# Optimization experiments

Hardware: AMD Instinct MI355X
Metric: run time of the kernel (lower is better)

## Reference

```python
import jax, jax.numpy as jnp
import numpy as np
from jax import lax

B, N, D, H, E, K, FF = 4, 1024, 1024, 16, 12, 2, 4
HD = D // H
EPS_LN = 1e-5


def setup_inputs() -> dict:
    key = jax.random.key(0)
    ks = jax.random.split(key, 10)
    s = 0.02
    return {
        "x": jax.random.normal(ks[0], (B, N, D), jnp.float32),
        "Wr": jax.random.normal(ks[1], (E, D), jnp.float32) * s,          # router [E, D] (no bias)
        "Wq": jax.random.normal(ks[2], (E, D, D), jnp.float32) * s,       # per-expert [out, in]
        "Wk": jax.random.normal(ks[3], (E, D, D), jnp.float32) * s,
        "Wv": jax.random.normal(ks[4], (E, D, D), jnp.float32) * s,
        "Wo": jax.random.normal(ks[5], (E, D, D), jnp.float32) * s,
        "W1": jax.random.normal(ks[6], (FF * D, D), jnp.float32) * s,
        "b1": jnp.zeros((FF * D,), jnp.float32),
        "W2": jax.random.normal(ks[7], (D, FF * D), jnp.float32) * s,
        "b2": jnp.zeros((D,), jnp.float32),
        "g1": jnp.ones((D,), jnp.float32),
        "be1": jnp.zeros((D,), jnp.float32),
        "g2": jnp.ones((D,), jnp.float32),
        "be2": jnp.zeros((D,), jnp.float32),
    }


def _ln(x, g, b):
    m = jnp.mean(x, axis=-1, keepdims=True)
    v = jnp.mean(jnp.square(x - m), axis=-1, keepdims=True)
    return (x - m) * lax.rsqrt(v + EPS_LN) * g + b


def _moe_mix(inp, W, combine):
    """sum_e combine[:, e] * (inp @ W[e].T) via scan over the E experts.
    inp: [T, Din], W: [E, Dout, Din], combine: [T, E] -> [T, Dout]"""
    def body(acc, ec):
        We, ce = ec
        return acc + ce[:, None] * (inp @ We.T), None
    acc0 = jnp.zeros((inp.shape[0], W.shape[1]), inp.dtype)
    acc, _ = lax.scan(body, acc0, (W, jnp.swapaxes(combine, 0, 1)))
    return acc


def _moe_attention(x, Wr, Wq, Wk, Wv, Wo):
    x_flat = x.reshape(-1, D)                     # [T, D]
    T = x_flat.shape[0]
    logits = x_flat @ Wr.T                        # [T, E]
    probs = jax.nn.softmax(logits, axis=-1)
    topv, topi = lax.top_k(probs, K)              # [T, K]
    topv = topv / (jnp.sum(topv, axis=-1, keepdims=True) + 1e-6)
    # dense combine weights [T, E] (zero for unselected experts)
    combine = jnp.zeros((T, E), x.dtype).at[jnp.arange(T)[:, None], topi].add(topv)

    q = _moe_mix(x_flat, Wq, combine)
    k = _moe_mix(x_flat, Wk, combine)
    v = _moe_mix(x_flat, Wv, combine)

    # [B, H, N, HD]
    q = q.reshape(B, N, H, HD).transpose(0, 2, 1, 3)
    k = k.reshape(B, N, H, HD).transpose(0, 2, 1, 3)
    v = v.reshape(B, N, H, HD).transpose(0, 2, 1, 3)
    scores = jnp.einsum("bhqd,bhkd->bhqk", q, k) / jnp.sqrt(jnp.asarray(HD, x.dtype))
    attn = jax.nn.softmax(scores, axis=-1)
    out = jnp.einsum("bhqk,bhkd->bhqd", attn, v)
    out_flat = out.transpose(0, 2, 1, 3).reshape(T, D)

    o = _moe_mix(out_flat, Wo, combine)           # expert output projection

    # load-balance loss (no grad in original: computed under torch.no_grad)
    counts = jnp.zeros((E,), x.dtype).at[topi.ravel()].add(1.0)
    p = probs.sum(axis=0)
    lb = jax.lax.stop_gradient((counts / (counts.sum() + 1e-6) * p).sum() * E)
    return o.reshape(B, N, D), lb


def reference(x, Wr, Wq, Wk, Wv, Wo, W1, b1, W2, b2, g1, be1, g2, be2):
    # pre-norm transformer block: x + MoEAttn(LN(x)); + FFN(LN(.))
    attn_out, lb = _moe_attention(_ln(x, g1, be1), Wr, Wq, Wk, Wv, Wo)
    h = x + attn_out
    hn = _ln(h, g2, be2)
    ff = (jax.nn.gelu(hn @ W1.T + b1)) @ W2.T + b2   # dropout=0 (eval)
    y = h + ff
    return y, lb
```

## Files before the change

### kernel.cpp

```cpp
#include <hip/hip_runtime.h>

#define B_ 4
#define N_ 1024
#define D_ 1024
#define H_ 16
#define HD_ 64
#define E_ 12
#define T_ 4096
#define FF_ 4096

static constexpr size_t SZ_ = (size_t)T_ * D_;

typedef __attribute__((ext_vector_type(8))) short bhalf8;
typedef __attribute__((ext_vector_type(4))) float f32x4;

#define GLDS(gp, lp)                                                         \
  __builtin_amdgcn_global_load_lds(                                          \
      (const __attribute__((address_space(1))) void*)(gp),                   \
      (__attribute__((address_space(3))) void*)(lp), 16, 0, 0)

__device__ __forceinline__ float wave_sum64(float v) {
#pragma unroll
  for (int o = 32; o > 0; o >>= 1) v += __shfl_down(v, o);
  return v;
}

__device__ __forceinline__ unsigned short f2bf(float f) {
  unsigned u = __float_as_uint(f);
  u += 0x7FFFu + ((u >> 16) & 1u);
  return (unsigned short)(u >> 16);
}
__device__ __forceinline__ float b2f(unsigned short s) {
  return __uint_as_float(((unsigned)s) << 16);
}
__device__ __forceinline__ unsigned addpair_bf(unsigned x, unsigned y) {
  float lo = b2f((unsigned short)(x & 0xffff)) + b2f((unsigned short)(y & 0xffff));
  float hi = b2f((unsigned short)(x >> 16)) + b2f((unsigned short)(y >> 16));
  return (unsigned)f2bf(lo) | ((unsigned)f2bf(hi) << 16);
}

__device__ __forceinline__ float gelu_f(float x) {
  float u = 0.7978845608028654f * (x + 0.044715f * x * x * x);
  u = fminf(fmaxf(u, -15.f), 15.f);
  float e = __expf(2.f * u);
  float th = (e - 1.f) / (e + 1.f);
  return 0.5f * x * (1.f + th);
}

__device__ __forceinline__ int slot_of(int row, int q) {
  return row * 4 + (q ^ ((row >> 1) & 3));
}

__global__ __launch_bounds__(256) void ln_kernel(const float* __restrict__ x,
    const float* __restrict__ g, const float* __restrict__ b,
    unsigned short* __restrict__ outb) {
  const int t = blockIdx.x, tid = threadIdx.x;
  const size_t base = (size_t)t * D_;
  const float4 v = ((const float4*)(x + base))[tid];
  float s = v.x + v.y + v.z + v.w;
  float s2 = v.x * v.x + v.y * v.y + v.z * v.z + v.w * v.w;
  s = wave_sum64(s);
  s2 = wave_sum64(s2);
  __shared__ float ls[4], ls2[4];
  const int w = tid >> 6;
  if ((tid & 63) == 0) { ls[w] = s; ls2[w] = s2; }
  __syncthreads();
  const float mean = (ls[0] + ls[1] + ls[2] + ls[3]) * (1.0f / D_);
  const float var = (ls2[0] + ls2[1] + ls2[2] + ls2[3]) * (1.0f / D_) - mean * mean;
  const float inv = rsqrtf(var + 1e-5f);
  const float4 gg = ((const float4*)g)[tid];
  const float4 bb = ((const float4*)b)[tid];
  ushort4 u4;
  u4.x = f2bf((v.x - mean) * inv * gg.x + bb.x);
  u4.y = f2bf((v.y - mean) * inv * gg.y + bb.y);
  u4.z = f2bf((v.z - mean) * inv * gg.z + bb.z);
  u4.w = f2bf((v.w - mean) * inv * gg.w + bb.w);
  ((ushort4*)(outb + base))[tid] = u4;
}

__global__ __launch_bounds__(256) void hln2_kernel(const float* __restrict__ x,
    const unsigned short* __restrict__ oa, const unsigned short* __restrict__ ob,
    const float* __restrict__ g, const float* __restrict__ be,
    const float* __restrict__ b2, float* __restrict__ y,
    unsigned short* __restrict__ hnb) {
  const int t = blockIdx.x, tid = threadIdx.x;
  const size_t base = (size_t)t * D_;
  const float4 xv = ((const float4*)(x + base))[tid];
  const ushort4 av = ((const ushort4*)(oa + base))[tid];
  const ushort4 bv = ((const ushort4*)(ob + base))[tid];
  float4 hv;
  hv.x = xv.x + b2f(av.x) + b2f(bv.x);
  hv.y = xv.y + b2f(av.y) + b2f(bv.y);
  hv.z = xv.z + b2f(av.z) + b2f(bv.z);
  hv.w = xv.w + b2f(av.w) + b2f(bv.w);
  const float4 b2v = ((const float4*)b2)[tid];
  float4 yv;
  yv.x = hv.x + b2v.x; yv.y = hv.y + b2v.y;
  yv.z = hv.z + b2v.z; yv.w = hv.w + b2v.w;
  ((float4*)(y + base))[tid] = yv;
  float s = hv.x + hv.y + hv.z + hv.w;
  float s2 = hv.x * hv.x + hv.y * hv.y + hv.z * hv.z + hv.w * hv.w;
  s = wave_sum64(s);
  s2 = wave_sum64(s2);
  __shared__ float ls[4], ls2[4];
  const int w = tid >> 6;
  if ((tid & 63) == 0) { ls[w] = s; ls2[w] = s2; }
  __syncthreads();
  const float mean = (ls[0] + ls[1] + ls[2] + ls[3]) * (1.0f / D_);
  const float var = (ls2[0] + ls2[1] + ls2[2] + ls2[3]) * (1.0f / D_) - mean * mean;
  const float inv = rsqrtf(var + 1e-5f);
  const float4 gg = ((const float4*)g)[tid];
  const float4 bb = ((const float4*)be)[tid];
  ushort4 o4;
  o4.x = f2bf((hv.x - mean) * inv * gg.x + bb.x);
  o4.y = f2bf((hv.y - mean) * inv * gg.y + bb.y);
  o4.z = f2bf((hv.z - mean) * inv * gg.z + bb.z);
  o4.w = f2bf((hv.w - mean) * inv * gg.w + bb.w);
  ((ushort4*)(hnb + base))[tid] = o4;
}

__global__ __launch_bounds__(256) void router_ln(const float* __restrict__ x,
    const float* __restrict__ g, const float* __restrict__ b,
    const float* __restrict__ Wr, float* __restrict__ probs,
    int* __restrict__ topi, float2* __restrict__ topw) {
  const int t = blockIdx.x, tid = threadIdx.x;
  const float4 xv = ((const float4*)(x + (size_t)t * D_))[tid];
  float s = xv.x + xv.y + xv.z + xv.w;
  float s2 = xv.x * xv.x + xv.y * xv.y + xv.z * xv.z + xv.w * xv.w;
  s = wave_sum64(s);
  s2 = wave_sum64(s2);
  __shared__ float ls[4], ls2[4];
  const int w = tid >> 6;
  if ((tid & 63) == 0) { ls[w] = s; ls2[w] = s2; }
  __syncthreads();
  const float mean = (ls[0] + ls[1] + ls[2] + ls[3]) * (1.0f / D_);
  const float var = (ls2[0] + ls2[1] + ls2[2] + ls2[3]) * (1.0f / D_) - mean * mean;
  const float inv = rsqrtf(var + 1e-5f);
  const float4 gg = ((const float4*)g)[tid];
  const float4 bb = ((const float4*)b)[tid];
  float4 xn4;
  xn4.x = (xv.x - mean) * inv * gg.x + bb.x;
  xn4.y = (xv.y - mean) * inv * gg.y + bb.y;
  xn4.z = (xv.z - mean) * inv * gg.z + bb.z;
  xn4.w = (xv.w - mean) * inv * gg.w + bb.w;
  float acc[E_];
#pragma unroll
  for (int e = 0; e < E_; ++e) {
    const float4 wv = ((const float4*)(Wr + (size_t)e * D_))[tid];
    acc[e] = xn4.x * wv.x + xn4.y * wv.y + xn4.z * wv.z + xn4.w * wv.w;
  }
#pragma unroll
  for (int e = 0; e < E_; ++e) acc[e] = wave_sum64(acc[e]);
  __shared__ float red[4][E_];
  if ((tid & 63) == 0) {
#pragma unroll
    for (int e = 0; e < E_; ++e) red[w][e] = acc[e];
  }
  __syncthreads();
  if (tid == 0) {
    float lg[E_];
    float mx = -1e30f;
#pragma unroll
    for (int e = 0; e < E_; ++e) {
      lg[e] = red[0][e] + red[1][e] + red[2][e] + red[3][e];
      mx = fmaxf(mx, lg[e]);
    }
    float p[E_];
    float sum = 0.f;
#pragma unroll
    for (int e = 0; e < E_; ++e) { p[e] = __expf(lg[e] - mx); sum += p[e]; }
    const float invs = 1.f / sum;
#pragma unroll
    for (int e = 0; e < E_; ++e) {
      p[e] *= invs;
      probs[t * E_ + e] = p[e];
    }
    int i0 = 0;
#pragma unroll
    for (int e = 1; e < E_; ++e) if (p[e] > p[i0]) i0 = e;
    int i1 = (i0 == 0) ? 1 : 0;
#pragma unroll
    for (int e = 0; e < E_; ++e) if (e != i0 && p[e] > p[i1]) i1 = e;
    const float rs = 1.f / (p[i0] + p[i1] + 1e-6f);
    topi[t] = i0 | (i1 << 8);
    topw[t] = make_float2(p[i0] * rs, p[i1] * rs);
  }
}

__global__ __launch_bounds__(256) void psum_kernel(const float* __restrict__ probs,
                                                   float* __restrict__ psum) {
  const int tid = threadIdx.x;
  float local[E_] = {};
  for (int t = tid; t < T_; t += 256) {
#pragma unroll
    for (int e = 0; e < E_; ++e) local[e] += probs[t * E_ + e];
  }
#pragma unroll
  for (int e = 0; e < E_; ++e) local[e] = wave_sum64(local[e]);
  __shared__ float red[4][E_];
  const int w = tid >> 6;
  if ((tid & 63) == 0) {
#pragma unroll
    for (int e = 0; e < E_; ++e) red[w][e] = local[e];
  }
  __syncthreads();
  if (tid < E_)
    psum[tid] = red[0][tid] + red[1][tid] + red[2][tid] + red[3][tid];
}

__global__ __launch_bounds__(256) void build_lists(const int* __restrict__ topi,
    const float2* __restrict__ topw, int* __restrict__ ecnt,
    int* __restrict__ etok, float* __restrict__ ewt) {
  const int e = blockIdx.x;
  const int tid = threadIdx.x;
  const int wid = tid >> 6, lane = tid & 63;
  __shared__ int wbase[4];
  __shared__ int base;
  if (tid == 0) base = 0;
  __syncthreads();
  for (int c = 0; c < T_; c += 256) {
    const int t = c + tid;
    const int pk = topi[t];
    const int i0 = pk & 0xFF, i1 = (pk >> 8) & 0xFF;
    const float2 w2 = topw[t];
    const int sel = (i0 == e) ? 0 : ((i1 == e) ? 1 : -1);
    const unsigned long long mask = __ballot(sel >= 0);
    const int prefix = __popcll(mask & ((1ULL << lane) - 1ULL));
    if (lane == 0) wbase[wid] = __popcll(mask);
    __syncthreads();
    if (tid == 0) {
      int s = base;
#pragma unroll
      for (int ww = 0; ww < 4; ++ww) { int cc = wbase[ww]; wbase[ww] = s; s += cc; }
      base = s;
    }
    __syncthreads();
    if (sel >= 0) {
      const int pos = wbase[wid] + prefix;
      etok[e * T_ + pos] = t | (sel << 16);
      ewt[e * T_ + pos] = sel ? w2.y : w2.x;
    }
    __syncthreads();
  }
  if (tid == 0) ecnt[e] = base;
}

__global__ __launch_bounds__(256) void cvtw_kernel(const float* __restrict__ src,
    unsigned short* __restrict__ dst) {
  const size_t i = (size_t)blockIdx.x * 256 + threadIdx.x;
  const float4 v = ((const float4*)src)[i];
  ushort4 o;
  o.x = f2bf(v.x); o.y = f2bf(v.y); o.z = f2bf(v.z); o.w = f2bf(v.w);
  ((ushort4*)dst)[i] = o;
}

__global__ __launch_bounds__(256) void cvtw3_kernel(const float* __restrict__ a,
    const float* __restrict__ b, const float* __restrict__ c,
    unsigned short* __restrict__ dst) {
  const int gw = (E_ * D_ * D_) / 1024;
  const int r = blockIdx.x / gw;
  const int ib = blockIdx.x - r * gw;
  const float* src = (r == 0) ? a : ((r == 1) ? b : c);
  const size_t i = (size_t)ib * 256 + threadIdx.x;
  const float4 v = ((const float4*)src)[i];
  ushort4 o;
  o.x = f2bf(v.x); o.y = f2bf(v.y); o.z = f2bf(v.z); o.w = f2bf(v.w);
  ((ushort4*)(dst + (size_t)r * E_ * D_ * D_))[i] = o;
}

__global__ __launch_bounds__(256) void moe_mfma(const unsigned short* __restrict__ Ab,
    const unsigned short* __restrict__ Wb, unsigned short* __restrict__ outb,
    const int* __restrict__ ecnt, const int* __restrict__ etok,
    const float* __restrict__ ewt) {
  const int e = blockIdx.z;
  const int Me = ecnt[e];
  const int m0 = blockIdx.y * 128;
  if (m0 >= Me) return;
  const int proj = blockIdx.x >> 3;
  const int n0 = (blockIdx.x & 7) * 128;
  const unsigned short* W = Wb + ((size_t)proj * E_ + e) * D_ * D_;
  unsigned short* out = outb + (size_t)proj * 2 * SZ_;
  __shared__ __align__(16) unsigned short As[128 * 32];
  __shared__ __align__(16) unsigned short Bs[128 * 32];
  __shared__ int stok[128];
  __shared__ float swt[128];
  const int tid = threadIdx.x;
  if (tid < 128) {
    const int s = m0 + tid;
    if (s < Me) { stok[tid] = etok[e * T_ + s]; swt[tid] = ewt[e * T_ + s]; }
    else        { stok[tid] = 0;                swt[tid] = 0.f; }
  }
  __syncthreads();
  const int s0 = tid, s1 = tid + 256;
  const int r0 = s0 >> 2, q0 = (s0 & 3) ^ ((r0 >> 1) & 3);
  const int r1 = s1 >> 2, q1 = (s1 & 3) ^ ((r1 >> 1) & 3);
  const unsigned short* aP0 = Ab + (size_t)(stok[r0] & 0xFFFF) * D_ + q0 * 8;
  const unsigned short* aP1 = Ab + (size_t)(stok[r1] & 0xFFFF) * D_ + q1 * 8;
  const unsigned short* bP0 = W + (size_t)(n0 + r0) * D_ + q0 * 8;
  const unsigned short* bP1 = W + (size_t)(n0 + r1) * D_ + q1 * 8;
  char* AsC = (char*)As;
  char* BsC = (char*)Bs;
  const int wave = tid >> 6, lane = tid & 63;
  const int wm0 = (wave >> 1) * 64, wn0 = (wave & 1) * 64;
  const int lr = lane & 15, lq = lane >> 4;
  int aoff[4], boff[4];
#pragma unroll
  for (int t = 0; t < 4; ++t) {
    aoff[t] = slot_of(wm0 + t * 16 + lr, lq) * 16;
    boff[t] = slot_of(wn0 + t * 16 + lr, lq) * 16;
  }
  f32x4 acc[4][4];
#pragma unroll
  for (int i = 0; i < 4; ++i)
#pragma unroll
    for (int j = 0; j < 4; ++j) acc[i][j] = (f32x4){0.f, 0.f, 0.f, 0.f};
  for (int kt = 0; kt < D_; kt += 32) {
    __syncthreads();
    GLDS(aP0 + kt, AsC + s0 * 16);
    GLDS(aP1 + kt, AsC + s1 * 16);
    GLDS(bP0 + kt, BsC + s0 * 16);
    GLDS(bP1 + kt, BsC + s1 * 16);
    __syncthreads();
    bhalf8 af[4], bfr[4];
#pragma unroll
    for (int t = 0; t < 4; ++t) af[t] = *(const bhalf8*)(AsC + aoff[t]);
#pragma unroll
    for (int t = 0; t < 4; ++t) bfr[t] = *(const bhalf8*)(BsC + boff[t]);
#pragma unroll
    for (int i = 0; i < 4; ++i)
#pragma unroll
      for (int j = 0; j < 4; ++j)
        acc[i][j] = __builtin_amdgcn_mfma_f32_16x16x32_bf16(af[i], bfr[j], acc[i][j], 0, 0, 0);
  }
#pragma unroll
  for (int mt = 0; mt < 4; ++mt)
#pragma unroll
    for (int nt = 0; nt < 4; ++nt) {
      const f32x4 c = acc[mt][nt];
      const int col = n0 + wn0 + nt * 16 + lr;
#pragma unroll
      for (int r = 0; r < 4; ++r) {
        const int row = wm0 + mt * 16 + lq * 4 + r;
        if (m0 + row < Me) {
          const int pk = stok[row];
          out[(size_t)(pk >> 16) * SZ_ + (size_t)(pk & 0xFFFF) * D_ + col] =
              f2bf(c[r] * swt[row]);
        }
      }
    }
}

__global__ __launch_bounds__(256) void ffn1_mfma(const unsigned short* __restrict__ Ab,
    const unsigned short* __restrict__ Bb, const float* __restrict__ bias,
    unsigned short* __restrict__ mid) {
  const int m0 = blockIdx.y * 128, n0 = blockIdx.x * 128;
  __shared__ __align__(16) unsigned short As[128 * 32];
  __shared__ __align__(16) unsigned short Bs[128 * 32];
  const int tid = threadIdx.x;
  const int s0 = tid, s1 = tid + 256;
  const int r0 = s0 >> 2, q0 = (s0 & 3) ^ ((r0 >> 1) & 3);
  const int r1 = s1 >> 2, q1 = (s1 & 3) ^ ((r1 >> 1) & 3);
  const unsigned short* aP0 = Ab + (size_t)(m0 + r0) * D_ + q0 * 8;
  const unsigned short* aP1 = Ab + (size_t)(m0 + r1) * D_ + q1 * 8;
  const unsigned short* bP0 = Bb + (size_t)(n0 + r0) * D_ + q0 * 8;
  const unsigned short* bP1 = Bb + (size_t)(n0 + r1) * D_ + q1 * 8;
  char* AsC = (char*)As;
  char* BsC = (char*)Bs;
  const int wave = tid >> 6, lane = tid & 63;
  const int wm0 = (wave >> 1) * 64, wn0 = (wave & 1) * 64;
  const int lr = lane & 15, lq = lane >> 4;
  int aoff[4], boff[4];
#pragma unroll
  for (int t = 0; t < 4; ++t) {
    aoff[t] = slot_of(wm0 + t * 16 + lr, lq) * 16;
    boff[t] = slot_of(wn0 + t * 16 + lr, lq) * 16;
  }
  f32x4 acc[4][4];
#pragma unroll
  for (int i = 0; i < 4; ++i)
#pragma unroll
    for (int j = 0; j < 4; ++j) acc[i][j] = (f32x4){0.f, 0.f, 0.f, 0.f};
  for (int kt = 0; kt < D_; kt += 32) {
    __syncthreads();
    GLDS(aP0 + kt, AsC + s0 * 16);
    GLDS(aP1 + kt, AsC + s1 * 16);
    GLDS(bP0 + kt, BsC + s0 * 16);
    GLDS(bP1 + kt, BsC + s1 * 16);
    __syncthreads();
    bhalf8 af[4], bfr[4];
#pragma unroll
    for (int t = 0; t < 4; ++t) af[t] = *(const bhalf8*)(AsC + aoff[t]);
#pragma unroll
    for (int t = 0; t < 4; ++t) bfr[t] = *(const bhalf8*)(BsC + boff[t]);
#pragma unroll
    for (int i = 0; i < 4; ++i)
#pragma unroll
      for (int j = 0; j < 4; ++j)
        acc[i][j] = __builtin_amdgcn_mfma_f32_16x16x32_bf16(af[i], bfr[j], acc[i][j], 0, 0, 0);
  }
  float bcol[4];
#pragma unroll
  for (int nt = 0; nt < 4; ++nt) bcol[nt] = bias[n0 + wn0 + nt * 16 + lr];
#pragma unroll
  for (int mt = 0; mt < 4; ++mt)
#pragma unroll
    for (int nt = 0; nt < 4; ++nt) {
      const f32x4 c = acc[mt][nt];
      const int col = n0 + wn0 + nt * 16 + lr;
#pragma unroll
      for (int r = 0; r < 4; ++r) {
        const int row = m0 + wm0 + mt * 16 + lq * 4 + r;
        mid[(size_t)row * FF_ + col] = f2bf(gelu_f(c[r] + bcol[nt]));
      }
    }
}

__global__ __launch_bounds__(256) void ffn2_split(const unsigned short* __restrict__ Ab,
    const unsigned short* __restrict__ Bb, float* __restrict__ part0,
    float* __restrict__ part1) {
  const int m0 = blockIdx.y * 128, n0 = blockIdx.x * 128;
  const int k0 = blockIdx.z * (FF_ / 2);
  float* const part = blockIdx.z ? part1 : part0;
  __shared__ __align__(16) unsigned short As[128 * 32];
  __shared__ __align__(16) unsigned short Bs[128 * 32];
  const int tid = threadIdx.x;
  const int s0 = tid, s1 = tid + 256;
  const int r0 = s0 >> 2, q0 = (s0 & 3) ^ ((r0 >> 1) & 3);
  const int r1 = s1 >> 2, q1 = (s1 & 3) ^ ((r1 >> 1) & 3);
  const unsigned short* aP0 = Ab + (size_t)(m0 + r0) * FF_ + q0 * 8 + k0;
  const unsigned short* aP1 = Ab + (size_t)(m0 + r1) * FF_ + q1 * 8 + k0;
  const unsigned short* bP0 = Bb + (size_t)(n0 + r0) * FF_ + q0 * 8 + k0;
  const unsigned short* bP1 = Bb + (size_t)(n0 + r1) * FF_ + q1 * 8 + k0;
  char* AsC = (char*)As;
  char* BsC = (char*)Bs;
  const int wave = tid >> 6, lane = tid & 63;
  const int wm0 = (wave >> 1) * 64, wn0 = (wave & 1) * 64;
  const int lr = lane & 15, lq = lane >> 4;
  int aoff[4], boff[4];
#pragma unroll
  for (int t = 0; t < 4; ++t) {
    aoff[t] = slot_of(wm0 + t * 16 + lr, lq) * 16;
    boff[t] = slot_of(wn0 + t * 16 + lr, lq) * 16;
  }
  f32x4 acc[4][4];
#pragma unroll
  for (int i = 0; i < 4; ++i)
#pragma unroll
    for (int j = 0; j < 4; ++j) acc[i][j] = (f32x4){0.f, 0.f, 0.f, 0.f};
  for (int kt = 0; kt < FF_ / 2; kt += 32) {
    __syncthreads();
    GLDS(aP0 + kt, AsC + s0 * 16);
    GLDS(aP1 + kt, AsC + s1 * 16);
    GLDS(bP0 + kt, BsC + s0 * 16);
    GLDS(bP1 + kt, BsC + s1 * 16);
    __syncthreads();
    bhalf8 af[4], bfr[4];
#pragma unroll
    for (int t = 0; t < 4; ++t) af[t] = *(const bhalf8*)(AsC + aoff[t]);
#pragma unroll
    for (int t = 0; t < 4; ++t) bfr[t] = *(const bhalf8*)(BsC + boff[t]);
#pragma unroll
    for (int i = 0; i < 4; ++i)
#pragma unroll
      for (int j = 0; j < 4; ++j)
        acc[i][j] = __builtin_amdgcn_mfma_f32_16x16x32_bf16(af[i], bfr[j], acc[i][j], 0, 0, 0);
  }
#pragma unroll
  for (int mt = 0; mt < 4; ++mt)
#pragma unroll
    for (int nt = 0; nt < 4; ++nt) {
      const f32x4 c = acc[mt][nt];
      const int col = n0 + wn0 + nt * 16 + lr;
#pragma unroll
      for (int r = 0; r < 4; ++r) {
        const int row = m0 + wm0 + mt * 16 + lq * 4 + r;
        part[(size_t)row * D_ + col] = c[r];
      }
    }
}

__global__ __launch_bounds__(256) void add3_kernel(float* __restrict__ y,
    const float* __restrict__ p0, const float* __restrict__ p1) {
  const size_t i = (size_t)blockIdx.x * 256 + threadIdx.x;
  const float4 a = ((const float4*)y)[i];
  const float4 u = ((const float4*)p0)[i];
  const float4 v = ((const float4*)p1)[i];
  float4 o;
  o.x = a.x + u.x + v.x;
  o.y = a.y + u.y + v.y;
  o.z = a.z + u.z + v.z;
  o.w = a.w + u.w + v.w;
  ((float4*)y)[i] = o;
}

__global__ __launch_bounds__(256) void add2b3_kernel(unsigned short* __restrict__ base) {
  const int reg = blockIdx.x >> 11;
  const int ib = blockIdx.x & 2047;
  unsigned short* a = base + (size_t)reg * 2 * SZ_;
  const unsigned short* b = a + SZ_;
  const size_t i = (size_t)ib * 256 + threadIdx.x;
  uint4 av = ((uint4*)a)[i];
  const uint4 bv = ((const uint4*)b)[i];
  av.x = addpair_bf(av.x, bv.x);
  av.y = addpair_bf(av.y, bv.y);
  av.z = addpair_bf(av.z, bv.z);
  av.w = addpair_bf(av.w, bv.w);
  ((uint4*)a)[i] = av;
}

__global__ __launch_bounds__(256) void attn_kernel(const unsigned short* __restrict__ q,
    const unsigned short* __restrict__ k, const unsigned short* __restrict__ v,
    unsigned short* __restrict__ out) {
  const int bh = blockIdx.x;
  const int b = bh >> 4, h = bh & 15;
  const int q0 = blockIdx.y * 64;
  const int tid = threadIdx.x;
  const int wave = tid >> 6, lane = tid & 63;
  const int lc = lane & 15, lg = lane >> 4;

  __shared__ __align__(16) unsigned short Ks[64 * 64];
  __shared__ __align__(16) unsigned short Vt[64 * 64];
  __shared__ __align__(16) unsigned short Pl[4][16 * 64];
  char* const KsC = (char*)Ks;
  char* const VtC = (char*)Vt;
  char* const PlC = (char*)&Pl[wave][0];

  bhalf8 qf0, qf1;
  {
    const unsigned short* qp =
        q + ((size_t)(b * N_ + q0 + wave * 16 + lc)) * D_ + h * HD_ + lg * 8;
    qf0 = *(const bhalf8*)qp;
    qf1 = *(const bhalf8*)(qp + 32);
  }

  int off[4][2];
#pragma unroll
  for (int t = 0; t < 4; ++t)
#pragma unroll
    for (int ch = 0; ch < 2; ++ch)
      off[t][ch] = (t * 16 + lc) * 128 + (((ch * 4 + lg) ^ (lc & 7)) << 4);

  const int krow = tid >> 2, ks0 = tid & 3;
  const unsigned short* const kgp =
      k + ((size_t)(b * N_ + krow)) * D_ + h * HD_ + ks0 * 8;
  const int kwo0 = krow * 128 + ((ks0 ^ (krow & 7)) << 4);
  const int kwo1 = krow * 128 + (((ks0 ^ 4) ^ (krow & 7)) << 4);
  const int vkv = (tid & 31) * 2, vd0 = (tid >> 5) * 8;
  const unsigned short* const vgp =
      v + ((size_t)(b * N_ + vkv)) * D_ + h * HD_ + vd0;
  int vwo[8];
#pragma unroll
  for (int c = 0; c < 8; ++c) {
    const int d = vd0 + c;
    vwo[c] = d * 128 + ((((vkv >> 3) ^ (d & 7)) << 4)) + (vkv & 7) * 2;
  }

  float m_i[4], l_i[4];
  f32x4 o_acc[4];
#pragma unroll
  for (int r = 0; r < 4; ++r) { m_i[r] = -3.0e38f; l_i[r] = 0.f; }
#pragma unroll
  for (int t = 0; t < 4; ++t) o_acc[t] = (f32x4){0.f, 0.f, 0.f, 0.f};

  uint4 ka = *(const uint4*)(kgp);
  uint4 kb = *(const uint4*)(kgp + 32);
  uint4 va = *(const uint4*)(vgp);
  uint4 vb = *(const uint4*)(vgp + D_);

  for (int kt = 0; kt < 16; ++kt) {
    __syncthreads();
    *(uint4*)(KsC + kwo0) = ka;
    *(uint4*)(KsC + kwo1) = kb;
    {
      const unsigned av4[4] = {va.x, va.y, va.z, va.w};
      const unsigned bv4[4] = {vb.x, vb.y, vb.z, vb.w};
#pragma unroll
      for (int c = 0; c < 4; ++c) {
        const unsigned w0 = (av4[c] & 0xffffu) | (bv4[c] << 16);
        const unsigned w1 = (av4[c] >> 16) | (bv4[c] & 0xffff0000u);
        *(unsigned*)(VtC + vwo[2 * c]) = w0;
        *(unsigned*)(VtC + vwo[2 * c + 1]) = w1;
      }
    }
    __syncthreads();
    if (kt < 15) {
      const size_t go = (size_t)(kt + 1) * 64 * D_;
      ka = *(const uint4*)(kgp + go);
      kb = *(const uint4*)(kgp + go + 32);
      va = *(const uint4*)(vgp + go);
      vb = *(const uint4*)(vgp + go + D_);
    }
    f32x4 s4[4];
#pragma unroll
    for (int t = 0; t < 4; ++t) {
      f32x4 acc = (f32x4){0.f, 0.f, 0.f, 0.f};
      acc = __builtin_amdgcn_mfma_f32_16x16x32_bf16(
          qf0, *(const bhalf8*)(KsC + off[t][0]), acc, 0, 0, 0);
      acc = __builtin_amdgcn_mfma_f32_16x16x32_bf16(
          qf1, *(const bhalf8*)(KsC + off[t][1]), acc, 0, 0, 0);
      s4[t] = acc;
    }
    float alpha[4];
#pragma unroll
    for (int r = 0; r < 4; ++r) {
      const float e0 = s4[0][r] * 0.125f, e1 = s4[1][r] * 0.125f;
      const float e2 = s4[2][r] * 0.125f, e3 = s4[3][r] * 0.125f;
      float mt = fmaxf(fmaxf(e0, e1), fmaxf(e2, e3));
#pragma unroll
      for (int o = 8; o > 0; o >>= 1) mt = fmaxf(mt, __shfl_xor(mt, o));
      const float mn = fmaxf(m_i[r], mt);
      alpha[r] = __expf(m_i[r] - mn);
      m_i[r] = mn;
      const float p0 = __expf(e0 - mn), p1 = __expf(e1 - mn);
      const float p2 = __expf(e2 - mn), p3 = __expf(e3 - mn);
      float rs = p0 + p1 + p2 + p3;
#pragma unroll
      for (int o = 8; o > 0; o >>= 1) rs += __shfl_xor(rs, o);
      l_i[r] = l_i[r] * alpha[r] + rs;
      const int qrow = 4 * lg + r;
      const int rb = qrow * 128 + (lc & 7) * 2;
      const int sw = qrow & 7;
      *(unsigned short*)(PlC + rb + (((0 + (lc >> 3)) ^ sw) << 4)) = f2bf(p0);
      *(unsigned short*)(PlC + rb + (((2 + (lc >> 3)) ^ sw) << 4)) = f2bf(p1);
      *(unsigned short*)(PlC + rb + (((4 + (lc >> 3)) ^ sw) << 4)) = f2bf(p2);
      *(unsigned short*)(PlC + rb + (((6 + (lc >> 3)) ^ sw) << 4)) = f2bf(p3);
    }
#pragma unroll
    for (int t = 0; t < 4; ++t) {
      f32x4 o = o_acc[t];
      o[0] *= alpha[0]; o[1] *= alpha[1]; o[2] *= alpha[2]; o[3] *= alpha[3];
      o_acc[t] = o;
    }
    const bhalf8 pf0 = *(const bhalf8*)(PlC + off[0][0]);
    const bhalf8 pf1 = *(const bhalf8*)(PlC + off[0][1]);
#pragma unroll
    for (int t = 0; t < 4; ++t) {
      o_acc[t] = __builtin_amdgcn_mfma_f32_16x16x32_bf16(
          pf0, *(const bhalf8*)(VtC + off[t][0]), o_acc[t], 0, 0, 0);
      o_acc[t] = __builtin_amdgcn_mfma_f32_16x16x32_bf16(
          pf1, *(const bhalf8*)(VtC + off[t][1]), o_acc[t], 0, 0, 0);
    }
  }
  const size_t obase = ((size_t)(b * N_ + q0 + wave * 16)) * D_ + h * HD_;
#pragma unroll
  for (int r = 0; r < 4; ++r) {
    const float inv = 1.f / l_i[r];
    const size_t rbase = obase + (size_t)(4 * lg + r) * D_;
#pragma unroll
    for (int t = 0; t < 4; ++t)
      out[rbase + t * 16 + lc] = f2bf(o_acc[t][r] * inv);
  }
}

__global__ void lb_kernel(const int* __restrict__ ecnt,
                          const float* __restrict__ psum, float* __restrict__ out) {
  if (threadIdx.x == 0 && blockIdx.x == 0) {
    float tot = 0.f;
    for (int e = 0; e < E_; ++e) tot += (float)ecnt[e];
    float s = 0.f;
    for (int e = 0; e < E_; ++e) s += (float)ecnt[e] / (tot + 1e-6f) * psum[e];
    out[0] = s * (float)E_;
  }
}

extern "C" void kernel_launch(void* const* d_in, const int* in_sizes, int n_in,
                              void* d_out, int out_size, void* d_ws, size_t ws_size,
                              hipStream_t stream) {
  (void)in_sizes; (void)n_in; (void)out_size;
  const float* x  = (const float*)d_in[0];
  const float* Wr = (const float*)d_in[1];
  const float* Wq = (const float*)d_in[2];
  const float* Wk = (const float*)d_in[3];
  const float* Wv = (const float*)d_in[4];
  const float* Wo = (const float*)d_in[5];
  const float* W1 = (const float*)d_in[6];
  const float* b1 = (const float*)d_in[7];
  const float* W2 = (const float*)d_in[8];
  const float* b2 = (const float*)d_in[9];
  const float* g1 = (const float*)d_in[10];
  const float* be1 = (const float*)d_in[11];
  const float* g2 = (const float*)d_in[12];
  const float* be2 = (const float*)d_in[13];
  float* y = (float*)d_out;

  const bool big = ws_size >= (size_t)136 * 1024 * 1024;
  char* p = (char*)d_ws;
  unsigned short *Rb, *xnb, *q2b, *WoB, *W1b, *W2b, *midb;
  char* tail;
  if (big) {
    Rb  = (unsigned short*)p;
    xnb = (unsigned short*)(p + 75497472);
    q2b = (unsigned short*)(p + 75497472 + 8388608);
    tail = p + 75497472 + 8388608 + 6 * SZ_ * 2;
    WoB  = Rb;
    W1b  = (unsigned short*)(p + 25165824);
    W2b  = (unsigned short*)(p + 33554432);
    midb = (unsigned short*)(p + 41943040);
  } else {
    Rb  = (unsigned short*)p;
    xnb = (unsigned short*)(p + 25165824);
    q2b = xnb + SZ_;
    W1b = q2b + 6 * SZ_;
    W2b = W1b + (size_t)FF_ * D_;
    tail = (char*)(W2b + (size_t)FF_ * D_);
    WoB  = Rb;
    midb = (unsigned short*)d_ws;
  }
  unsigned short* k2b = q2b + 2 * SZ_;
  unsigned short* v2b = k2b + 2 * SZ_;
  float* psum = (float*)tail;            tail += E_ * 4;
  int* ecnt = (int*)tail;                tail += E_ * 4;
  int* etok = (int*)tail;                tail += (size_t)E_ * T_ * 4;
  float* ewt = (float*)tail;             tail += (size_t)E_ * T_ * 4;
  float* probs = (float*)tail;           tail += (size_t)T_ * E_ * 4;
  int* topi = (int*)tail;                tail += T_ * 4;
  float2* topw = (float2*)tail;
  unsigned short* attb = v2b + SZ_;
  unsigned short* o2b  = q2b;
  unsigned short* hnb  = v2b;
  float* part0         = (float*)k2b;
  float* part1         = (float*)v2b;

  const int gw = (E_ * D_ * D_) / 1024;
  ln_kernel<<<T_, 256, 0, stream>>>(x, g1, be1, xnb);
  router_ln<<<T_, 256, 0, stream>>>(x, g1, be1, Wr, probs, topi, topw);
  psum_kernel<<<1, 256, 0, stream>>>(probs, psum);
  build_lists<<<E_, 256, 0, stream>>>(topi, topw, ecnt, etok, ewt);
  if (big) {
    cvtw3_kernel<<<3 * gw, 256, 0, stream>>>(Wq, Wk, Wv, Rb);
    moe_mfma<<<dim3(24, T_ / 128, E_), 256, 0, stream>>>(xnb, Rb, q2b, ecnt, etok, ewt);
    cvtw_kernel<<<gw, 256, 0, stream>>>(Wo, WoB);
    cvtw_kernel<<<(FF_ * D_) / 1024, 256, 0, stream>>>(W1, W1b);
    cvtw_kernel<<<(FF_ * D_) / 1024, 256, 0, stream>>>(W2, W2b);
  } else {
    cvtw_kernel<<<(FF_ * D_) / 1024, 256, 0, stream>>>(W1, W1b);
    cvtw_kernel<<<(FF_ * D_) / 1024, 256, 0, stream>>>(W2, W2b);
    cvtw_kernel<<<gw, 256, 0, stream>>>(Wq, Rb);
    moe_mfma<<<dim3(8, T_ / 128, E_), 256, 0, stream>>>(xnb, Rb, q2b, ecnt, etok, ewt);
    cvtw_kernel<<<gw, 256, 0, stream>>>(Wk, Rb);
    moe_mfma<<<dim3(8, T_ / 128, E_), 256, 0, stream>>>(xnb, Rb, k2b, ecnt, etok, ewt);
    cvtw_kernel<<<gw, 256, 0, stream>>>(Wv, Rb);
    moe_mfma<<<dim3(8, T_ / 128, E_), 256, 0, stream>>>(xnb, Rb, v2b, ecnt, etok, ewt);
    cvtw_kernel<<<gw, 256, 0, stream>>>(Wo, Rb);
  }
  add2b3_kernel<<<3 * (SZ_ / 2048), 256, 0, stream>>>(q2b);
  attn_kernel<<<dim3(B_ * H_, N_ / 64), 256, 0, stream>>>(q2b, k2b, v2b, attb);
  moe_mfma<<<dim3(8, T_ / 128, E_), 256, 0, stream>>>(attb, WoB, o2b, ecnt, etok, ewt);
  hln2_kernel<<<T_, 256, 0, stream>>>(x, o2b, o2b + SZ_, g2, be2, b2, y, hnb);
  ffn1_mfma<<<dim3(FF_ / 128, T_ / 128), 256, 0, stream>>>(hnb, W1b, b1, midb);
  ffn2_split<<<dim3(D_ / 128, T_ / 128, 2), 256, 0, stream>>>(midb, W2b, part0, part1);
  add3_kernel<<<SZ_ / 1024, 256, 0, stream>>>(y, part0, part1);
  lb_kernel<<<1, 64, 0, stream>>>(ecnt, psum, y + SZ_);
}
```

Baseline: 627.7 us.

## Triple-buffer LDS in MFMA GEMMs and fuse LN1 into router kernel

```diff
diff --git a/kernel.cpp b/kernel.cpp
--- a/kernel.cpp
+++ b/kernel.cpp
@@ -51,32 +51,51 @@
   return row * 4 + (q ^ ((row >> 1) & 3));
 }
 
-__global__ __launch_bounds__(256) void ln_kernel(const float* __restrict__ x,
-    const float* __restrict__ g, const float* __restrict__ b,
-    unsigned short* __restrict__ outb) {
-  const int t = blockIdx.x, tid = threadIdx.x;
-  const size_t base = (size_t)t * D_;
-  const float4 v = ((const float4*)(x + base))[tid];
-  float s = v.x + v.y + v.z + v.w;
-  float s2 = v.x * v.x + v.y * v.y + v.z * v.z + v.w * v.w;
-  s = wave_sum64(s);
-  s2 = wave_sum64(s2);
-  __shared__ float ls[4], ls2[4];
-  const int w = tid >> 6;
-  if ((tid & 63) == 0) { ls[w] = s; ls2[w] = s2; }
-  __syncthreads();
-  const float mean = (ls[0] + ls[1] + ls[2] + ls[3]) * (1.0f / D_);
-  const float var = (ls2[0] + ls2[1] + ls2[2] + ls2[3]) * (1.0f / D_) - mean * mean;
-  const float inv = rsqrtf(var + 1e-5f);
-  const float4 gg = ((const float4*)g)[tid];
-  const float4 bb = ((const float4*)b)[tid];
-  ushort4 u4;
-  u4.x = f2bf((v.x - mean) * inv * gg.x + bb.x);
-  u4.y = f2bf((v.y - mean) * inv * gg.y + bb.y);
-  u4.z = f2bf((v.z - mean) * inv * gg.z + bb.z);
-  u4.w = f2bf((v.w - mean) * inv * gg.w + bb.w);
-  ((ushort4*)(outb + base))[tid] = u4;
-}
+#define GEMM_PHASE(u, NPH_)                                                  \
+  {                                                                          \
+    const int p_ = kp + (u);                                                 \
+    const int kpre_ = (p_ + 2) * 32;                                         \
+    char* const cA_ = (char*)As[(u)];                                        \
+    char* const cB_ = (char*)Bs[(u)];                                        \
+    char* const pA_ = (char*)As[((u) + 2) % 3];                              \
+    char* const pB_ = (char*)Bs[((u) + 2) % 3];                              \
+    if (kpre_ < (NPH_)*32) {                                                 \
+      GLDS(aP0 + kpre_, pA_ + s0 * 16);                                      \
+      GLDS(aP1 + kpre_, pA_ + s1 * 16);                                      \
+      GLDS(bP0 + kpre_, pB_ + s0 * 16);                                      \
+      GLDS(bP1 + kpre_, pB_ + s1 * 16);                                      \
+    }                                                                        \
+    const int rem_ = (NPH_)-1 - p_;                                          \
+    if (rem_ >= 2)                                                           \
+      asm volatile("s_waitcnt vmcnt(8)" ::: "memory");                       \
+    else if (rem_ == 1)                                                      \
+      asm volatile("s_waitcnt vmcnt(4)" ::: "memory");                       \
+    else                                                                     \
+      asm volatile("s_waitcnt vmcnt(0)" ::: "memory");                       \
+    asm volatile("s_barrier" ::: "memory");                                  \
+    bhalf8 af_[4], bf_[4];                                                   \
+    _Pragma("unroll") for (int t = 0; t < 4; ++t) af_[t] =                   \
+        *(const bhalf8*)(cA_ + aoff[t]);                                     \
+    _Pragma("unroll") for (int t = 0; t < 4; ++t) bf_[t] =                   \
+        *(const bhalf8*)(cB_ + boff[t]);                                     \
+    __builtin_amdgcn_s_setprio(1);                                           \
+    _Pragma("unroll") for (int i = 0; i < 4; ++i)                            \
+        _Pragma("unroll") for (int j = 0; j < 4; ++j) acc[i][j] =            \
+        __builtin_amdgcn_mfma_f32_16x16x32_bf16(af_[i], bf_[j], acc[i][j],   \
+                                                0, 0, 0);                    \
+    __builtin_amdgcn_s_setprio(0);                                           \
+    asm volatile("s_barrier" ::: "memory");                                  \
+  }
+
+#define GEMM_PROLOGUE()                                                      \
+  GLDS(aP0, (char*)As[0] + s0 * 16);                                         \
+  GLDS(aP1, (char*)As[0] + s1 * 16);                                         \
+  GLDS(bP0, (char*)Bs[0] + s0 * 16);                                         \
+  GLDS(bP1, (char*)Bs[0] + s1 * 16);                                         \
+  GLDS(aP0 + 32, (char*)As[1] + s0 * 16);                                    \
+  GLDS(aP1 + 32, (char*)As[1] + s1 * 16);                                    \
+  GLDS(bP0 + 32, (char*)Bs[1] + s0 * 16);                                    \
+  GLDS(bP1 + 32, (char*)Bs[1] + s1 * 16);
 
 __global__ __launch_bounds__(256) void hln2_kernel(const float* __restrict__ x,
     const unsigned short* __restrict__ oa, const unsigned short* __restrict__ ob,
@@ -121,8 +140,8 @@
 
 __global__ __launch_bounds__(256) void router_ln(const float* __restrict__ x,
     const float* __restrict__ g, const float* __restrict__ b,
-    const float* __restrict__ Wr, float* __restrict__ probs,
-    int* __restrict__ topi, float2* __restrict__ topw) {
+    const float* __restrict__ Wr, unsigned short* __restrict__ xnb,
+    float* __restrict__ probs, int* __restrict__ topi, float2* __restrict__ topw) {
   const int t = blockIdx.x, tid = threadIdx.x;
   const float4 xv = ((const float4*)(x + (size_t)t * D_))[tid];
   float s = xv.x + xv.y + xv.z + xv.w;
@@ -143,6 +162,10 @@
   xn4.y = (xv.y - mean) * inv * gg.y + bb.y;
   xn4.z = (xv.z - mean) * inv * gg.z + bb.z;
   xn4.w = (xv.w - mean) * inv * gg.w + bb.w;
+  ushort4 u4;
+  u4.x = f2bf(xn4.x); u4.y = f2bf(xn4.y);
+  u4.z = f2bf(xn4.z); u4.w = f2bf(xn4.w);
+  ((ushort4*)(xnb + (size_t)t * D_))[tid] = u4;
   float acc[E_];
 #pragma unroll
   for (int e = 0; e < E_; ++e) {
@@ -280,8 +303,8 @@
   const int n0 = (blockIdx.x & 7) * 128;
   const unsigned short* W = Wb + ((size_t)proj * E_ + e) * D_ * D_;
   unsigned short* out = outb + (size_t)proj * 2 * SZ_;
-  __shared__ __align__(16) unsigned short As[128 * 32];
-  __shared__ __align__(16) unsigned short Bs[128 * 32];
+  __shared__ __align__(16) unsigned short As[3][128 * 32];
+  __shared__ __align__(16) unsigned short Bs[3][128 * 32];
   __shared__ int stok[128];
   __shared__ float swt[128];
   const int tid = threadIdx.x;
@@ -298,8 +321,6 @@
   const unsigned short* aP1 = Ab + (size_t)(stok[r1] & 0xFFFF) * D_ + q1 * 8;
   const unsigned short* bP0 = W + (size_t)(n0 + r0) * D_ + q0 * 8;
   const unsigned short* bP1 = W + (size_t)(n0 + r1) * D_ + q1 * 8;
-  char* AsC = (char*)As;
-  char* BsC = (char*)Bs;
   const int wave = tid >> 6, lane = tid & 63;
   const int wm0 = (wave >> 1) * 64, wn0 = (wave & 1) * 64;
   const int lr = lane & 15, lq = lane >> 4;
@@ -314,23 +335,11 @@
   for (int i = 0; i < 4; ++i)
 #pragma unroll
     for (int j = 0; j < 4; ++j) acc[i][j] = (f32x4){0.f, 0.f, 0.f, 0.f};
-  for (int kt = 0; kt < D_; kt += 32) {
-    __syncthreads();
-    GLDS(aP0 + kt, AsC + s0 * 16);
-    GLDS(aP1 + kt, AsC + s1 * 16);
-    GLDS(bP0 + kt, BsC + s0 * 16);
-    GLDS(bP1 + kt, BsC + s1 * 16);
-    __syncthreads();
-    bhalf8 af[4], bfr[4];
-#pragma unroll
-    for (int t = 0; t < 4; ++t) af[t] = *(const bhalf8*)(AsC + aoff[t]);
-#pragma unroll
-    for (int t = 0; t < 4; ++t) bfr[t] = *(const bhalf8*)(BsC + boff[t]);
-#pragma unroll
-    for (int i = 0; i < 4; ++i)
-#pragma unroll
-      for (int j = 0; j < 4; ++j)
-        acc[i][j] = __builtin_amdgcn_mfma_f32_16x16x32_bf16(af[i], bfr[j], acc[i][j], 0, 0, 0);
+  GEMM_PROLOGUE()
+  for (int kp = 0; kp < 32; kp += 3) {
+    GEMM_PHASE(0, 32)
+    if (kp + 1 < 32) GEMM_PHASE(1, 32)
+    if (kp + 2 < 32) GEMM_PHASE(2, 32)
   }
 #pragma unroll
   for (int mt = 0; mt < 4; ++mt)
@@ -354,8 +363,8 @@
     const unsigned short* __restrict__ Bb, const float* __restrict__ bias,
     unsigned short* __restrict__ mid) {
   const int m0 = blockIdx.y * 128, n0 = blockIdx.x * 128;
-  __shared__ __align__(16) unsigned short As[128 * 32];
-  __shared__ __align__(16) unsigned short Bs[128 * 32];
+  __shared__ __align__(16) unsigned short As[3][128 * 32];
+  __shared__ __align__(16) unsigned short Bs[3][128 * 32];
   const int tid = threadIdx.x;
   const int s0 = tid, s1 = tid + 256;
   const int r0 = s0 >> 2, q0 = (s0 & 3) ^ ((r0 >> 1) & 3);
@@ -364,8 +373,6 @@
   const unsigned short* aP1 = Ab + (size_t)(m0 + r1) * D_ + q1 * 8;
   const unsigned short* bP0 = Bb + (size_t)(n0 + r0) * D_ + q0 * 8;
   const unsigned short* bP1 = Bb + (size_t)(n0 + r1) * D_ + q1 * 8;
-  char* AsC = (char*)As;
-  char* BsC = (char*)Bs;
   const int wave = tid >> 6, lane = tid & 63;
   const int wm0 = (wave >> 1) * 64, wn0 = (wave & 1) * 64;
   const int lr = lane & 15, lq = lane >> 4;
@@ -380,23 +387,11 @@
   for (int i = 0; i < 4; ++i)
 #pragma unroll
     for (int j = 0; j < 4; ++j) acc[i][j] = (f32x4){0.f, 0.f, 0.f, 0.f};
-  for (int kt = 0; kt < D_; kt += 32) {
-    __syncthreads();
-    GLDS(aP0 + kt, AsC + s0 * 16);
-    GLDS(aP1 + kt, AsC + s1 * 16);
-    GLDS(bP0 + kt, BsC + s0 * 16);
-    GLDS(bP1 + kt, BsC + s1 * 16);
-    __syncthreads();
-    bhalf8 af[4], bfr[4];
-#pragma unroll
-    for (int t = 0; t < 4; ++t) af[t] = *(const bhalf8*)(AsC + aoff[t]);
-#pragma unroll
-    for (int t = 0; t < 4; ++t) bfr[t] = *(const bhalf8*)(BsC + boff[t]);
-#pragma unroll
-    for (int i = 0; i < 4; ++i)
-#pragma unroll
-      for (int j = 0; j < 4; ++j)
-        acc[i][j] = __builtin_amdgcn_mfma_f32_16x16x32_bf16(af[i], bfr[j], acc[i][j], 0, 0, 0);
+  GEMM_PROLOGUE()
+  for (int kp = 0; kp < 32; kp += 3) {
+    GEMM_PHASE(0, 32)
+    if (kp + 1 < 32) GEMM_PHASE(1, 32)
+    if (kp + 2 < 32) GEMM_PHASE(2, 32)
   }
   float bcol[4];
 #pragma unroll
@@ -421,8 +416,8 @@
   const int m0 = blockIdx.y * 128, n0 = blockIdx.x * 128;
   const int k0 = blockIdx.z * (FF_ / 2);
   float* const part = blockIdx.z ? part1 : part0;
-  __shared__ __align__(16) unsigned short As[128 * 32];
-  __shared__ __align__(16) unsigned short Bs[128 * 32];
+  __shared__ __align__(16) unsigned short As[3][128 * 32];
+  __shared__ __align__(16) unsigned short Bs[3][128 * 32];
   const int tid = threadIdx.x;
   const int s0 = tid, s1 = tid + 256;
   const int r0 = s0 >> 2, q0 = (s0 & 3) ^ ((r0 >> 1) & 3);
@@ -431,8 +426,6 @@
   const unsigned short* aP1 = Ab + (size_t)(m0 + r1) * FF_ + q1 * 8 + k0;
   const unsigned short* bP0 = Bb + (size_t)(n0 + r0) * FF_ + q0 * 8 + k0;
   const unsigned short* bP1 = Bb + (size_t)(n0 + r1) * FF_ + q1 * 8 + k0;
-  char* AsC = (char*)As;
-  char* BsC = (char*)Bs;
   const int wave = tid >> 6, lane = tid & 63;
   const int wm0 = (wave >> 1) * 64, wn0 = (wave & 1) * 64;
   const int lr = lane & 15, lq = lane >> 4;
@@ -447,23 +440,11 @@
   for (int i = 0; i < 4; ++i)
 #pragma unroll
     for (int j = 0; j < 4; ++j) acc[i][j] = (f32x4){0.f, 0.f, 0.f, 0.f};
-  for (int kt = 0; kt < FF_ / 2; kt += 32) {
-    __syncthreads();
-    GLDS(aP0 + kt, AsC + s0 * 16);
-    GLDS(aP1 + kt, AsC + s1 * 16);
-    GLDS(bP0 + kt, BsC + s0 * 16);
-    GLDS(bP1 + kt, BsC + s1 * 16);
-    __syncthreads();
-    bhalf8 af[4], bfr[4];
-#pragma unroll
-    for (int t = 0; t < 4; ++t) af[t] = *(const bhalf8*)(AsC + aoff[t]);
-#pragma unroll
-    for (int t = 0; t < 4; ++t) bfr[t] = *(const bhalf8*)(BsC + boff[t]);
-#pragma unroll
-    for (int i = 0; i < 4; ++i)
-#pragma unroll
-      for (int j = 0; j < 4; ++j)
-        acc[i][j] = __builtin_amdgcn_mfma_f32_16x16x32_bf16(af[i], bfr[j], acc[i][j], 0, 0, 0);
+  GEMM_PROLOGUE()
+  for (int kp = 0; kp < 64; kp += 3) {
+    GEMM_PHASE(0, 64)
+    if (kp + 1 < 64) GEMM_PHASE(1, 64)
+    if (kp + 2 < 64) GEMM_PHASE(2, 64)
   }
 #pragma unroll
   for (int mt = 0; mt < 4; ++mt)
@@ -722,8 +703,7 @@
   float* part1         = (float*)v2b;
 
   const int gw = (E_ * D_ * D_) / 1024;
-  ln_kernel<<<T_, 256, 0, stream>>>(x, g1, be1, xnb);
-  router_ln<<<T_, 256, 0, stream>>>(x, g1, be1, Wr, probs, topi, topw);
+  router_ln<<<T_, 256, 0, stream>>>(x, g1, be1, Wr, xnb, probs, topi, topw);
   psum_kernel<<<1, 256, 0, stream>>>(probs, psum);
   build_lists<<<E_, 256, 0, stream>>>(topi, topw, ecnt, etok, ewt);
   if (big) {
```

Measured after the change: 616.9 us. About the same (-1.7%).
